# Optimization experiments

Measured on AMD Instinct MI355X. Metric: run time of the kernel, lower is better.

## Reference

```python
import jax, jax.numpy as jnp
import numpy as np


def setup_inputs() -> dict:
    key = jax.random.key(0)
    ks = jax.random.split(key, 6)
    B, S, H, F, E = 4, 2048, 1024, 4096, 8
    x = jax.random.normal(ks[0], (B, S, H), dtype=jnp.float32)
    Wr = jax.random.normal(ks[1], (H, E), dtype=jnp.float32) * (1.0 / np.sqrt(H))
    br = jnp.zeros((E,), dtype=jnp.float32)
    W1 = jax.random.normal(ks[2], (E, H, F), dtype=jnp.float32) * (1.0 / np.sqrt(H))
    b1 = jnp.zeros((E, F), dtype=jnp.float32)
    W2 = jax.random.normal(ks[3], (E, F, H), dtype=jnp.float32) * (1.0 / np.sqrt(F))
    b2 = jnp.zeros((E, H), dtype=jnp.float32)
    b_buf = jnp.zeros((E,), dtype=jnp.float32)  # load-balancing bias buffer, zero-init
    return {"x": x, "b_buf": b_buf, "Wr": Wr, "br": br,
            "W1": W1, "b1": b1, "W2": W2, "b2": b2, "k": 2}


def reference(x, b_buf, Wr, br, W1, b1, W2, b2, k):
    # Router
    scores = jnp.einsum('bsh,he->bse', x, Wr) + br          # [B,S,E]
    probs = jax.nn.softmax(scores, axis=-1)
    # load_balancing: expert selection uses biased scores (b_buf pre-update)
    _, expert_id = jax.lax.top_k(probs + b_buf, k)          # [B,S,k] int
    # combine weights use unbiased probs
    p, _ = jax.lax.top_k(probs, k)                          # [B,S,k]
    # Dense-dispatch reference: run every expert MLP on all tokens,
    # then select via one-hot mask (same math as gather/scatter dispatch).
    h1 = jnp.einsum('bsh,ehf->ebsf', x, W1) + b1[:, None, None, :]
    h1 = jax.nn.gelu(h1, approximate=False)                 # torch nn.GELU = exact
    out_e = jnp.einsum('ebsf,efh->ebsh', h1, W2) + b2[:, None, None, :]
    E = W1.shape[0]
    onehot = (expert_id[None, :, :, :] == jnp.arange(E)[:, None, None, None]).astype(x.dtype)  # [E,B,S,k]
    out_k = jnp.einsum('ebsk,ebsh->bskh', onehot, out_e)    # scatter-combine per slot
    w = p / jnp.sum(p, axis=-1, keepdims=True)              # normalize top-k probs
    return jnp.einsum('bsk,bskh->bsh', w, out_k)
```

## Files before the change

kernel.cpp:

```cpp
#include <hip/hip_runtime.h>
#include <stdint.h>

#define NTOK 8192
#define H_ 1024
#define F_ 4096
#define E_ 8
#define VCAP 18432
#define VMBLK 72
#define NCOMP 16384

using f32x4  = __attribute__((ext_vector_type(4))) float;
using short8 = __attribute__((ext_vector_type(8))) short;

typedef __attribute__((address_space(1))) const uint32_t gu32;
typedef __attribute__((address_space(3))) uint32_t lu32;

__device__ __forceinline__ void glds16(const void* g, void* l) {
  __builtin_amdgcn_global_load_lds((gu32*)g, (lu32*)l, 16, 0, 0);
}

__device__ __forceinline__ ushort f2bf(float f) {
  union { float f; uint32_t u; } v; v.f = f;
  uint32_t r = (v.u + 0x7FFFu + ((v.u >> 16) & 1u)) >> 16;
  return (ushort)r;
}

__device__ __forceinline__ float gelu_t(float x) {
  float u = 0.7978845608028654f * (x + 0.044715f * x * x * x);
  float e = exp2f(u * 2.885390081777927f);
  float th = 1.0f - 2.0f / (1.0f + e);
  return 0.5f * x * (1.0f + th);
}

__global__ void k_init(int* cnt, int* cur, int* tok, float* wl, int* v2c) {
  int i = blockIdx.x * 256 + threadIdx.x;
  if (i < E_) { cnt[i] = 0; cur[i] = 0; }
  if (i < VCAP) { tok[i] = -1; wl[i] = 0.f; v2c[i] = -1; }
}

__global__ __launch_bounds__(256) void k_transcvt(const float* __restrict__ W,
                                                  ushort* __restrict__ WT,
                                                  int R, int C) {
  __shared__ float t[64][65];
  int e = blockIdx.z;
  int c0 = blockIdx.x * 64, r0 = blockIdx.y * 64;
  const float* Wp = W + (size_t)e * R * C;
  ushort* Tp = WT + (size_t)e * R * C;
  int tx = threadIdx.x & 15, ty = threadIdx.x >> 4;
#pragma unroll
  for (int i = 0; i < 4; i++) {
    int lr = ty + i * 16;
    const float4 v = *(const float4*)&Wp[(size_t)(r0 + lr) * C + c0 + tx * 4];
    t[lr][tx * 4 + 0] = v.x; t[lr][tx * 4 + 1] = v.y;
    t[lr][tx * 4 + 2] = v.z; t[lr][tx * 4 + 3] = v.w;
  }
  __syncthreads();
#pragma unroll
  for (int i = 0; i < 4; i++) {
    int lc = ty + i * 16;
    ushort4 o;
    o.x = f2bf(t[tx * 4 + 0][lc]);
    o.y = f2bf(t[tx * 4 + 1][lc]);
    o.z = f2bf(t[tx * 4 + 2][lc]);
    o.w = f2bf(t[tx * 4 + 3][lc]);
    *(ushort4*)&Tp[(size_t)(c0 + lc) * R + r0 + tx * 4] = o;
  }
}

__global__ __launch_bounds__(256) void k_router(const float* __restrict__ x,
                                                const float* __restrict__ Wr,
                                                const float* __restrict__ br,
                                                const float* __restrict__ bbuf,
                                                int* cnt, int* te, float* tw) {
  int wid = threadIdx.x >> 6, lane = threadIdx.x & 63;
  int t = blockIdx.x * 4 + wid;
  const float* xp = x + (size_t)t * H_;
  double acc[E_];
#pragma unroll
  for (int e = 0; e < E_; e++) acc[e] = 0.0;
  for (int j = lane; j < H_; j += 64) {
    float xv = xp[j];
    const float4 w0 = *(const float4*)&Wr[j * 8];
    const float4 w1 = *(const float4*)&Wr[j * 8 + 4];
    acc[0] += (double)xv * (double)w0.x;
    acc[1] += (double)xv * (double)w0.y;
    acc[2] += (double)xv * (double)w0.z;
    acc[3] += (double)xv * (double)w0.w;
    acc[4] += (double)xv * (double)w1.x;
    acc[5] += (double)xv * (double)w1.y;
    acc[6] += (double)xv * (double)w1.z;
    acc[7] += (double)xv * (double)w1.w;
  }
#pragma unroll
  for (int e = 0; e < E_; e++)
    for (int s = 32; s > 0; s >>= 1) acc[e] += __shfl_xor(acc[e], s);
  if (lane == 0) {
    double s[E_], m = -1e300;
    for (int e = 0; e < E_; e++) { s[e] = acc[e] + (double)br[e]; if (s[e] > m) m = s[e]; }
    double pe[E_], sum = 0.0;
    for (int e = 0; e < E_; e++) { pe[e] = exp(s[e] - m); sum += pe[e]; }
    double pr[E_], bb[E_];
    for (int e = 0; e < E_; e++) { pr[e] = pe[e] / sum; bb[e] = pr[e] + (double)bbuf[e]; }
    int e0 = 0;
    for (int e = 1; e < E_; e++) if (bb[e] > bb[e0]) e0 = e;
    int e1 = (e0 == 0) ? 1 : 0;
    for (int e = 0; e < E_; e++) if (e != e0 && bb[e] > bb[e1]) e1 = e;
    int a0 = 0;
    for (int e = 1; e < E_; e++) if (pr[e] > pr[a0]) a0 = e;
    int a1 = (a0 == 0) ? 1 : 0;
    for (int e = 0; e < E_; e++) if (e != a0 && pr[e] > pr[a1]) a1 = e;
    double iv = 1.0 / (pr[a0] + pr[a1]);
    te[t * 2] = e0; te[t * 2 + 1] = e1;
    tw[t * 2] = (float)(pr[a0] * iv); tw[t * 2 + 1] = (float)(pr[a1] * iv);
    atomicAdd(&cnt[e0], 1); atomicAdd(&cnt[e1], 1);
  }
}

__global__ void k_offsets(const int* cnt, int* off, int* coff) {
  if (threadIdx.x == 0 && blockIdx.x == 0) {
    int o = 0, c = 0;
    for (int e = 0; e < E_; e++) {
      off[e] = o; coff[e] = c;
      o += ((cnt[e] + 255) >> 8) << 8;
      c += cnt[e];
    }
    off[E_] = o; coff[E_] = c;
  }
}

__global__ void k_build(const int* __restrict__ te, const float* __restrict__ tw,
                        const int* __restrict__ off, const int* __restrict__ coff,
                        int* cur, int* tok, float* wl, int* v2c, int* ctok) {
  int t = blockIdx.x * 256 + threadIdx.x;
  if (t >= NTOK) return;
#pragma unroll
  for (int s = 0; s < 2; s++) {
    int e = te[t * 2 + s];
    int slot = atomicAdd(&cur[e], 1);
    int vp = off[e] + slot;
    int cp = coff[e] + slot;
    tok[vp] = t; wl[vp] = tw[t * 2 + s]; v2c[vp] = cp; ctok[cp] = t;
  }
}

__global__ __launch_bounds__(256) void k_gather(const float* __restrict__ x,
                                                const int* __restrict__ ctok,
                                                ushort* __restrict__ Xg) {
  int row = blockIdx.x;
  int t = ctok[row];
  const float4* src = (const float4*)(x + (size_t)t * H_);
  ushort4* dst = (ushort4*)(Xg + (size_t)row * H_);
  int i = threadIdx.x;
  float4 v = src[i];
  ushort4 o; o.x = f2bf(v.x); o.y = f2bf(v.y); o.z = f2bf(v.z); o.w = f2bf(v.w);
  dst[i] = o;
}

__global__ void k_zero(float* out) {
  size_t i = (size_t)blockIdx.x * 256 + threadIdx.x;
  float4 z; z.x = 0.f; z.y = 0.f; z.z = 0.f; z.w = 0.f;
  ((float4*)out)[i] = z;
}

template <int MODE>
__global__ __launch_bounds__(512) void k_gemm(const ushort* __restrict__ A,
                                              const ushort* __restrict__ BT,
                                              const float* __restrict__ bias,
                                              ushort* __restrict__ h1,
                                              float* __restrict__ Out,
                                              const int* __restrict__ off,
                                              const int* __restrict__ v2c,
                                              const int* __restrict__ tok,
                                              const float* __restrict__ wl,
                                              int K, int N, int NTe) {
  extern __shared__ char lds[];
  int nwg = gridDim.x;
  int cpx = nwg >> 3;
  int bid = blockIdx.x;
  int lid = (bid & 7) * cpx + (bid >> 3);
  int gsz = NTe << 2;
  int g = lid / gsz, rm = lid % gsz;
  int ne = rm >> 2, m = (g << 2) + (rm & 3);
  int row0 = m << 8;
  if (row0 >= off[E_]) return;
  int e = 0;
  while (off[e + 1] <= row0) e++;
  int n0, k0, nk;
  if (MODE == 0) { n0 = ne << 8; k0 = 0; nk = K >> 6; }
  else           { n0 = (ne >> 1) << 8; k0 = (ne & 1) * (K >> 1); nk = K >> 7; }
  const ushort* Bp = BT + (size_t)e * (size_t)N * (size_t)K;

  int tid = threadIdx.x, lane = tid & 63, w = tid >> 6;
  int wr = w >> 2, wc = w & 3;

  f32x4 acc[8][4];
#pragma unroll
  for (int mm = 0; mm < 8; mm++)
#pragma unroll
    for (int nn = 0; nn < 4; nn++) acc[mm][nn] = (f32x4){0.f, 0.f, 0.f, 0.f};

  int urow = (w << 3) + (lane >> 3);
  int schunk = (lane & 7) ^ (lane >> 3);
  const char *aS0, *aS1, *aS2, *aS3, *bS0, *bS1, *bS2, *bS3;
  {
    int v0 = v2c[row0 + 0 * 64 + urow];   if (v0 < 0) v0 = 0;
    int v1 = v2c[row0 + 1 * 64 + urow];   if (v1 < 0) v1 = 0;
    int v2 = v2c[row0 + 2 * 64 + urow];   if (v2 < 0) v2 = 0;
    int v3 = v2c[row0 + 3 * 64 + urow];   if (v3 < 0) v3 = 0;
    size_t kb = (size_t)k0 * 2 + (size_t)schunk * 16;
    aS0 = (const char*)(A + (size_t)v0 * K) + kb;
    aS1 = (const char*)(A + (size_t)v1 * K) + kb;
    aS2 = (const char*)(A + (size_t)v2 * K) + kb;
    aS3 = (const char*)(A + (size_t)v3 * K) + kb;
    bS0 = (const char*)(Bp + (size_t)(n0 + 0 * 64 + urow) * K) + kb;
    bS1 = (const char*)(Bp + (size_t)(n0 + 1 * 64 + urow) * K) + kb;
    bS2 = (const char*)(Bp + (size_t)(n0 + 2 * 64 + urow) * K) + kb;
    bS3 = (const char*)(Bp + (size_t)(n0 + 3 * 64 + urow) * K) + kb;
  }

  int fr = lane & 15, fq = lane >> 4;
  int frs = fr & 7;

  short8 af_[4][2], bf_[2][2];

#define STG_A(u, tt, bbuf) glds16(aS##u + (size_t)(tt) * 128, lds + (bbuf) * 65536 + (u) * 8192 + (w << 10))
#define STG_B(u, tt, bbuf) glds16(bS##u + (size_t)(tt) * 128, lds + (bbuf) * 65536 + 32768 + (u) * 8192 + (w << 10))

#define RDA(mmq, bbuf) do {                                                  \
    const ushort* LA_ = (const ushort*)(lds + (bbuf) * 65536);               \
    _Pragma("unroll")                                                        \
    for (int i = 0; i < 4; ++i)                                              \
      _Pragma("unroll")                                                      \
      for (int ks = 0; ks < 2; ++ks)                                         \
        af_[i][ks] = *(const short8*)&LA_[((wr << 7) + ((mmq) + i) * 16 + fr) * 64 + (((ks << 2) + fq) ^ frs) * 8]; \
  } while (0)

#define RDB(nnq, bbuf) do {                                                  \
    const ushort* LB_ = (const ushort*)(lds + (bbuf) * 65536 + 32768);       \
    _Pragma("unroll")                                                        \
    for (int i = 0; i < 2; ++i)                                              \
      _Pragma("unroll")                                                      \
      for (int ks = 0; ks < 2; ++ks)                                         \
        bf_[i][ks] = *(const short8*)&LB_[((wc << 6) + ((nnq) + i) * 16 + fr) * 64 + (((ks << 2) + fq) ^ frs) * 8]; \
  } while (0)

#define MMQ(mmq, nnq) do {                                                   \
    __builtin_amdgcn_s_setprio(1);                                           \
    _Pragma("unroll")                                                        \
    for (int i = 0; i < 4; ++i)                                              \
      _Pragma("unroll")                                                      \
      for (int jn = 0; jn < 2; ++jn)                                         \
        _Pragma("unroll")                                                    \
        for (int ks = 0; ks < 2; ++ks)                                       \
          acc[(mmq) + i][(nnq) + jn] = __builtin_amdgcn_mfma_f32_16x16x32_bf16(af_[i][ks], bf_[jn][ks], acc[(mmq) + i][(nnq) + jn], 0, 0, 0); \
    __builtin_amdgcn_s_setprio(0);                                           \
  } while (0)

#define FENCE() __builtin_amdgcn_sched_barrier(0)
#define BAR()   __builtin_amdgcn_s_barrier()

  STG_B(0, 0, 0); STG_B(1, 0, 0); STG_B(2, 0, 0); STG_B(3, 0, 0);
  STG_A(0, 0, 0); STG_A(2, 0, 0); STG_A(1, 0, 0); STG_A(3, 0, 0);
  asm volatile("s_waitcnt vmcnt(2)" ::: "memory");
  BAR(); FENCE();

  for (int t = 0; t < nk; ++t) {
    int bb = t & 1, nb = bb ^ 1;
    bool pre = (t + 1 < nk);
    if (pre) { STG_B(0, t + 1, nb); STG_B(1, t + 1, nb); }
    RDB(0, bb); RDA(0, bb);
    MMQ(0, 0);
    FENCE();
    if (pre) asm volatile("s_waitcnt vmcnt(2)" ::: "memory");
    else     asm volatile("s_waitcnt vmcnt(0)" ::: "memory");
    BAR(); FENCE();
    if (pre) { STG_B(2, t + 1, nb); STG_B(3, t + 1, nb); }
    RDA(4, bb);
    MMQ(4, 0);
    FENCE(); BAR(); FENCE();
    if (pre) { STG_A(0, t + 1, nb); STG_A(2, t + 1, nb); }
    RDB(2, bb);
    MMQ(4, 2);
    FENCE(); BAR(); FENCE();
    if (pre) { STG_A(1, t + 1, nb); STG_A(3, t + 1, nb); }
    RDA(0, bb);
    MMQ(0, 2);
    FENCE();
    if (pre) asm volatile("s_waitcnt vmcnt(2)" ::: "memory");
    BAR(); FENCE();
  }
#undef STG_A
#undef STG_B
#undef RDA
#undef RDB
#undef MMQ
#undef FENCE
#undef BAR

  const float* bp = bias + (size_t)e * N;
  int cb = n0 + (wc << 6);
  if (MODE == 0) {
#pragma unroll
    for (int mm = 0; mm < 8; mm++) {
#pragma unroll
      for (int j = 0; j < 4; j++) {
        int vr = row0 + (wr << 7) + mm * 16 + (fq << 2) + j;
        int cr = v2c[vr];
        if (cr < 0) continue;
        ushort* hp = h1 + (size_t)cr * N + cb;
#pragma unroll
        for (int nn = 0; nn < 4; nn++) {
          float v = acc[mm][nn][j] + bp[cb + nn * 16 + fr];
          hp[nn * 16 + fr] = f2bf(gelu_t(v));
        }
      }
    }
  } else {
    bool addb = (k0 == 0);
#pragma unroll
    for (int mm = 0; mm < 8; mm++) {
#pragma unroll
      for (int j = 0; j < 4; j++) {
        int vr = row0 + (wr << 7) + mm * 16 + (fq << 2) + j;
        int t2 = tok[vr];
        if (t2 < 0) continue;
        float wgt = wl[vr];
#pragma unroll
        for (int nn = 0; nn < 4; nn++) {
          int c = cb + nn * 16 + fr;
          float v = acc[mm][nn][j] + (addb ? bp[c] : 0.f);
          atomicAdd(&Out[(size_t)t2 * (size_t)N + c], wgt * v);
        }
      }
    }
  }
}

extern "C" void kernel_launch(void* const* d_in, const int* in_sizes, int n_in,
                              void* d_out, int out_size, void* d_ws, size_t ws_size,
                              hipStream_t stream) {
  (void)in_sizes; (void)n_in; (void)out_size; (void)ws_size;
  const float* x    = (const float*)d_in[0];
  const float* bbuf = (const float*)d_in[1];
  const float* Wr   = (const float*)d_in[2];
  const float* br   = (const float*)d_in[3];
  const float* W1   = (const float*)d_in[4];
  const float* b1   = (const float*)d_in[5];
  const float* W2   = (const float*)d_in[6];
  const float* b2   = (const float*)d_in[7];
  float* out = (float*)d_out;

  char* ws = (char*)d_ws;
  ushort* W1T = (ushort*)ws;
  ushort* W2T = (ushort*)(ws + 67108864);
  ushort* Xg  = (ushort*)(ws + 134217728);
  ushort* h1  = (ushort*)(ws + 167772160);
  char* meta  = ws + 301989888;
  int*   cnt  = (int*)(meta);
  int*   off  = (int*)(meta + 64);
  int*   coff = (int*)(meta + 128);
  int*   cur  = (int*)(meta + 192);
  int*   te   = (int*)(meta + 256);
  float* tw   = (float*)(meta + 65792);
  int*   tok  = (int*)(meta + 131328);
  float* wl   = (float*)(meta + 205056);
  int*   v2c  = (int*)(meta + 278784);
  int*   ctok = (int*)(meta + 352512);

  hipFuncSetAttribute((const void*)&k_gemm<0>,
                      hipFuncAttributeMaxDynamicSharedMemorySize, 131072);
  hipFuncSetAttribute((const void*)&k_gemm<1>,
                      hipFuncAttributeMaxDynamicSharedMemorySize, 131072);

  k_init<<<VMBLK, 256, 0, stream>>>(cnt, cur, tok, wl, v2c);
  k_transcvt<<<dim3(F_ / 64, H_ / 64, E_), 256, 0, stream>>>(W1, W1T, H_, F_);
  k_transcvt<<<dim3(H_ / 64, F_ / 64, E_), 256, 0, stream>>>(W2, W2T, F_, H_);
  k_router<<<NTOK / 4, 256, 0, stream>>>(x, Wr, br, bbuf, cnt, te, tw);
  k_offsets<<<1, 64, 0, stream>>>(cnt, off, coff);
  k_build<<<NTOK / 256, 256, 0, stream>>>(te, tw, off, coff, cur, tok, wl, v2c, ctok);
  k_gather<<<NCOMP, 256, 0, stream>>>(x, ctok, Xg);
  k_zero<<<(NTOK * H_ / 4) / 256, 256, 0, stream>>>(out);
  k_gemm<0><<<16 * VMBLK, 512, 131072, stream>>>(Xg, W1T, b1, h1, nullptr,
                                                 off, v2c, nullptr, nullptr,
                                                 H_, F_, 16);
  k_gemm<1><<<8 * VMBLK, 512, 131072, stream>>>(h1, W2T, b2, nullptr, out,
                                                off, v2c, tok, wl,
                                                F_, H_, 8);
}
```

Before: 1.004 ms.

## Deepen GEMM prefetch to two k-tiles ahead and load full B fragments once

Restructures the MFMA main loop so global-to-LDS loads are issued two k-iterations ahead instead of one, spread between MFMA quads. All B fragments are read from LDS once per iteration into a larger register array, which replaces the earlier split reads. The loop drops from four barriers per iteration to three and adds explicit lgkmcnt waits. The aim is to hide more global memory latency and cut LDS reads, at the cost of more vector registers and tighter buffer-reuse ordering.

New measurement: 998.5 us. No clear change (-0.6%).

```diff
diff --git a/kernel.cpp b/kernel.cpp
--- a/kernel.cpp
+++ b/kernel.cpp
@@ -221,7 +221,7 @@
   int fr = lane & 15, fq = lane >> 4;
   int frs = fr & 7;
 
-  short8 af_[4][2], bf_[2][2];
+  short8 af_[4][2], bf_[4][2];
 
 #define STG_A(u, tt, bbuf) glds16(aS##u + (size_t)(tt) * 128, lds + (bbuf) * 65536 + (u) * 8192 + (w << 10))
 #define STG_B(u, tt, bbuf) glds16(bS##u + (size_t)(tt) * 128, lds + (bbuf) * 65536 + 32768 + (u) * 8192 + (w << 10))
@@ -235,13 +235,13 @@
         af_[i][ks] = *(const short8*)&LA_[((wr << 7) + ((mmq) + i) * 16 + fr) * 64 + (((ks << 2) + fq) ^ frs) * 8]; \
   } while (0)
 
-#define RDB(nnq, bbuf) do {                                                  \
+#define RDB(bbuf) do {                                                       \
     const ushort* LB_ = (const ushort*)(lds + (bbuf) * 65536 + 32768);       \
     _Pragma("unroll")                                                        \
-    for (int i = 0; i < 2; ++i)                                              \
+    for (int i = 0; i < 4; ++i)                                              \
       _Pragma("unroll")                                                      \
       for (int ks = 0; ks < 2; ++ks)                                         \
-        bf_[i][ks] = *(const short8*)&LB_[((wc << 6) + ((nnq) + i) * 16 + fr) * 64 + (((ks << 2) + fq) ^ frs) * 8]; \
+        bf_[i][ks] = *(const short8*)&LB_[((wc << 6) + i * 16 + fr) * 64 + (((ks << 2) + fq) ^ frs) * 8]; \
   } while (0)
 
 #define MMQ(mmq, nnq) do {                                                   \
@@ -252,42 +252,41 @@
       for (int jn = 0; jn < 2; ++jn)                                         \
         _Pragma("unroll")                                                    \
         for (int ks = 0; ks < 2; ++ks)                                       \
-          acc[(mmq) + i][(nnq) + jn] = __builtin_amdgcn_mfma_f32_16x16x32_bf16(af_[i][ks], bf_[jn][ks], acc[(mmq) + i][(nnq) + jn], 0, 0, 0); \
+          acc[(mmq) + i][(nnq) + jn] = __builtin_amdgcn_mfma_f32_16x16x32_bf16(af_[i][ks], bf_[(nnq) + jn][ks], acc[(mmq) + i][(nnq) + jn], 0, 0, 0); \
     __builtin_amdgcn_s_setprio(0);                                           \
   } while (0)
 
 #define FENCE() __builtin_amdgcn_sched_barrier(0)
 #define BAR()   __builtin_amdgcn_s_barrier()
+#define WAIT_LGKM() asm volatile("s_waitcnt lgkmcnt(0)" ::: "memory")
 
   STG_B(0, 0, 0); STG_B(1, 0, 0); STG_B(2, 0, 0); STG_B(3, 0, 0);
-  STG_A(0, 0, 0); STG_A(2, 0, 0); STG_A(1, 0, 0); STG_A(3, 0, 0);
-  asm volatile("s_waitcnt vmcnt(2)" ::: "memory");
-  BAR(); FENCE();
-
-  for (int t = 0; t < nk; ++t) {
-    int bb = t & 1, nb = bb ^ 1;
-    bool pre = (t + 1 < nk);
-    if (pre) { STG_B(0, t + 1, nb); STG_B(1, t + 1, nb); }
-    RDB(0, bb); RDA(0, bb);
+  STG_A(0, 0, 0); STG_A(1, 0, 0); STG_A(2, 0, 0); STG_A(3, 0, 0);
+  if (nk > 1) {
+    STG_B(0, 1, 1); STG_B(1, 1, 1); STG_B(2, 1, 1); STG_B(3, 1, 1);
+    STG_A(0, 1, 1); STG_A(2, 1, 1);
+  }
+
+  for (int T = 0; T < nk; ++T) {
+    int bb = T & 1, nb = bb ^ 1;
+    bool s1 = (T + 1 < nk), s2 = (T + 2 < nk);
+    if (s1) { STG_A(1, T + 1, nb); STG_A(3, T + 1, nb); }
+    if (s1) asm volatile("s_waitcnt vmcnt(8)" ::: "memory");
+    else    asm volatile("s_waitcnt vmcnt(0)" ::: "memory");
+    BAR(); FENCE();
+    RDA(0, bb); RDB(bb);
+    WAIT_LGKM(); FENCE();
+    BAR(); FENCE();
     MMQ(0, 0);
-    FENCE();
-    if (pre) asm volatile("s_waitcnt vmcnt(2)" ::: "memory");
-    else     asm volatile("s_waitcnt vmcnt(0)" ::: "memory");
+    if (s2) { STG_B(0, T + 2, bb); STG_B(1, T + 2, bb); }
+    MMQ(0, 2);
+    if (s2) { STG_B(2, T + 2, bb); STG_B(3, T + 2, bb); }
+    RDA(4, bb);
+    WAIT_LGKM(); FENCE();
     BAR(); FENCE();
-    if (pre) { STG_B(2, t + 1, nb); STG_B(3, t + 1, nb); }
-    RDA(4, bb);
     MMQ(4, 0);
-    FENCE(); BAR(); FENCE();
-    if (pre) { STG_A(0, t + 1, nb); STG_A(2, t + 1, nb); }
-    RDB(2, bb);
+    if (s2) { STG_A(0, T + 2, bb); STG_A(2, T + 2, bb); }
     MMQ(4, 2);
-    FENCE(); BAR(); FENCE();
-    if (pre) { STG_A(1, t + 1, nb); STG_A(3, t + 1, nb); }
-    RDA(0, bb);
-    MMQ(0, 2);
-    FENCE();
-    if (pre) asm volatile("s_waitcnt vmcnt(2)" ::: "memory");
-    BAR(); FENCE();
   }
 #undef STG_A
 #undef STG_B
@@ -296,6 +295,7 @@
 #undef MMQ
 #undef FENCE
 #undef BAR
+#undef WAIT_LGKM
 
   const float* bp = bias + (size_t)e * N;
   int cb = n0 + (wc << 6);
```
